# Kernel tuning notes

Measured on AMD Instinct MI355X. Metric: run time of the kernel, lower is better.

The kernel has to match this reference:

```python
import jax, jax.numpy as jnp
import numpy as np

EPS = 0.5          # residual scaling (module __init__ eps)
N = 100_000        # num nodes
E = 1_250_000      # num edges (avg degree ~12.5)
D = 64             # feature dim


def setup_inputs() -> dict:
    key = jax.random.key(0)
    k1, k2, k3 = jax.random.split(key, 3)
    x = jax.random.normal(k1, (N, D), dtype=jnp.float32)
    src = jax.random.randint(k2, (E,), 0, N, dtype=jnp.int32)
    dst = jax.random.randint(k3, (E,), 0, N, dtype=jnp.int32)
    return {"x": x, "src": src, "dst": dst}


def reference(x, src, dst):
    n = x.shape[0]
    # out-degree of each node = number of edges with that node as source
    deg = jax.ops.segment_sum(jnp.ones(src.shape, dtype=x.dtype), src, num_segments=n)
    norm = jnp.power(jnp.maximum(deg, 1.0), -0.5)          # [N]
    edge_norm = norm[src] * norm[dst]                      # [E] (u_mul_v)
    msg = x[src] * edge_norm[:, None]                      # [E, D] (u_mul_e)
    h = jax.ops.segment_sum(msg, dst, num_segments=n)      # sum per destination
    return h + x * EPS
```

## Files before the change

kernel.cpp:

```cpp
#include <hip/hip_runtime.h>

constexpr int D        = 64;
constexpr float EPS    = 0.5f;
constexpr int BKT      = 128;
constexpr int CAPB_MAX = 2048;
constexpr int EPB      = 4096;
constexpr int NBMAX    = 1024;
constexpr int MAXOVF   = 65536;

__device__ __forceinline__ unsigned int f2bf(float f) {
    unsigned int u = __float_as_uint(f);
    return (u + 0x7FFFu + ((u >> 16) & 1u)) >> 16;
}
__device__ __forceinline__ float bf2f_lo(unsigned int v) { return __uint_as_float(v << 16); }
__device__ __forceinline__ float bf2f_hi(unsigned int v) { return __uint_as_float(v & 0xFFFF0000u); }


__global__ void init_kernel(int* __restrict__ curD, int* __restrict__ curS,
                            int* __restrict__ ovf_cnt, int* __restrict__ sovf_cnt,
                            int NB, int capb) {
    int i = blockIdx.x * blockDim.x + threadIdx.x;
    if (i < NB) { curD[i] = i * capb; curS[i] = i * capb; }
    if (i == 0) { *ovf_cnt = 0; *sovf_cnt = 0; }
}

__global__ __launch_bounds__(256)
void partition_kernel(const int* __restrict__ src, const int* __restrict__ dst,
                      int* __restrict__ curD, int* __restrict__ curS,
                      unsigned int* __restrict__ rec, unsigned char* __restrict__ srec,
                      int* __restrict__ ovf_cnt, int* __restrict__ ovf,
                      int* __restrict__ sovf_cnt, int* __restrict__ sovf,
                      int E, int NB, int capb) {
    __shared__ int histD[NBMAX];
    __shared__ int histS[NBMAX];
    __shared__ int startD[NBMAX];
    __shared__ int startS[NBMAX];
    const int base = blockIdx.x * EPB;
    const int tid  = threadIdx.x;
    for (int b = tid; b < NB; b += 256) { histD[b] = 0; histS[b] = 0; }
    __syncthreads();

    #pragma unroll
    for (int k = 0; k < EPB / 256; ++k) {
        int e = base + tid + k * 256;
        if (e < E) {
            atomicAdd(&histD[dst[e] >> 7], 1);
            atomicAdd(&histS[src[e] >> 7], 1);
        }
    }
    __syncthreads();
    for (int b = tid; b < NB; b += 256) {
        int c = histD[b];
        startD[b] = (c > 0) ? atomicAdd(&curD[b], c) : 0;
        histD[b] = 0;
        int c2 = histS[b];
        startS[b] = (c2 > 0) ? atomicAdd(&curS[b], c2) : 0;
        histS[b] = 0;
    }
    __syncthreads();
    #pragma unroll
    for (int k = 0; k < EPB / 256; ++k) {
        int e = base + tid + k * 256;
        if (e < E) {
            int s = src[e], t = dst[e];
            int bD = t >> 7;
            int r  = atomicAdd(&histD[bD], 1);
            int pD = startD[bD] + r;
            if (pD < (bD + 1) * capb) {
                rec[pD] = ((unsigned int)s << 7) | (unsigned int)(t & (BKT - 1));
            } else {
                int i = atomicAdd(ovf_cnt, 1);
                if (i < MAXOVF) { ovf[2 * i] = s; ovf[2 * i + 1] = t; }
            }
            int bS = s >> 7;
            int r2 = atomicAdd(&histS[bS], 1);
            int pS = startS[bS] + r2;
            if (pS < (bS + 1) * capb) {
                srec[pS] = (unsigned char)(s & (BKT - 1));
            } else {
                int i = atomicAdd(sovf_cnt, 1);
                if (i < MAXOVF) sovf[i] = s;
            }
        }
    }
}

__global__ __launch_bounds__(256)
void combo_kernel(const unsigned int* __restrict__ rec, const unsigned char* __restrict__ srec,
                  const int* __restrict__ curD, const int* __restrict__ curS,
                  int* __restrict__ csr, int* __restrict__ row_start,
                  int* __restrict__ row_cnt, const float2* __restrict__ x2,
                  float* __restrict__ norm, unsigned int* __restrict__ yh,
                  const int* __restrict__ sovf_cnt, const int* __restrict__ sovf,
                  int n, int NB, int capb) {
    __shared__ unsigned int recs[CAPB_MAX];
    __shared__ int srcs[CAPB_MAX];
    __shared__ int hist[BKT];
    __shared__ int scanv[BKT];
    __shared__ int rankb[BKT];
    __shared__ float nrm[BKT];
    const int tid = threadIdx.x;

    if (blockIdx.x >= NB) {
        int b = blockIdx.x - NB;
        int cnt = curS[b] - b * capb;
        if (cnt > capb) cnt = capb;
        if (tid < BKT) hist[tid] = 0;
        __syncthreads();
        for (int i = tid; i < cnt; i += 256)
            atomicAdd(&hist[srec[(size_t)b * capb + i]], 1);
        __syncthreads();
        int oc = *sovf_cnt;
        if (oc > 0) {
            if (oc > MAXOVF) oc = MAXOVF;
            for (int i = tid; i < oc; i += 256) {
                int s = sovf[i];
                if ((s >> 7) == b) atomicAdd(&hist[s & (BKT - 1)], 1);
            }
            __syncthreads();
        }
        if (tid < BKT) {
            int node = b * BKT + tid;
            float nm = rsqrtf(fmaxf((float)hist[tid], 1.0f));
            nrm[tid] = nm;
            if (node < n) norm[node] = nm;
        }
        __syncthreads();
        int nodes = n - b * BKT;
        if (nodes > BKT) nodes = BKT;
        if (nodes < 0) nodes = 0;
        int total = nodes * (D / 2);
        size_t gbase = (size_t)b * BKT * (D / 2);
        for (int i = tid; i < total; i += 256) {
            float2 v = x2[gbase + i];
            float nm = nrm[i >> 5];
            yh[gbase + i] = f2bf(v.x * nm) | (f2bf(v.y * nm) << 16);
        }
        return;
    }

    const int b = blockIdx.x;
    int cnt = curD[b] - b * capb;
    if (cnt > capb) cnt = capb;
    for (int i = tid; i < cnt; i += 256) recs[i] = rec[(size_t)b * capb + i];
    if (tid < BKT) hist[tid] = 0;
    __syncthreads();
    for (int i = tid; i < cnt; i += 256) atomicAdd(&hist[recs[i] & (BKT - 1)], 1);
    __syncthreads();
    if (tid < BKT) scanv[tid] = hist[tid];
    __syncthreads();
    #pragma unroll
    for (int off = 1; off < BKT; off <<= 1) {
        int t = 0;
        if (tid < BKT && tid >= off) t = scanv[tid - off];
        __syncthreads();
        if (tid < BKT) scanv[tid] += t;
        __syncthreads();
    }
    if (tid < BKT) {
        int excl = scanv[tid] - hist[tid];
        rankb[tid] = excl;
        int node = b * BKT + tid;
        if (node < n) {
            row_start[node] = b * capb + excl;
            row_cnt[node]   = hist[tid];
        }
    }
    __syncthreads();
    for (int i = tid; i < cnt; i += 256) {
        unsigned int v = recs[i];
        int pos = atomicAdd(&rankb[v & (BKT - 1)], 1);
        srcs[pos] = (int)(v >> 7);
    }
    __syncthreads();
    for (int i = tid; i < cnt; i += 256) csr[(size_t)b * capb + i] = srcs[i];
}

__global__ __launch_bounds__(256)
void gather8_kernel(const uint4* __restrict__ yr4, const float4* __restrict__ x4,
                    const int* __restrict__ csr, const int* __restrict__ row_start,
                    const int* __restrict__ row_cnt, const float* __restrict__ norm,
                    float4* __restrict__ out4, int n) {
    int wid  = (blockIdx.x * blockDim.x + threadIdx.x) >> 6;
    int lane = threadIdx.x & 63;
    int fl   = lane & 7;
    int node = wid * 8 + (lane >> 3);
    bool valid = node < n;
    int rs  = valid ? row_start[node] : 0;
    int cnt = valid ? row_cnt[node] : 0;
    int m = cnt;
    m = max(m, __shfl_xor(m, 8));
    m = max(m, __shfl_xor(m, 16));
    m = max(m, __shfl_xor(m, 32));
    float a0 = 0.f, a1 = 0.f, a2 = 0.f, a3 = 0.f, a4 = 0.f, a5 = 0.f, a6 = 0.f, a7 = 0.f;
    for (int k = 0; k < m; k += 4) {
        #pragma unroll
        for (int j = 0; j < 4; ++j) {
            int kj = k + j;
            bool take = kj < cnt;
            int s = csr[rs + (take ? kj : 0)];
            s = take ? s : 0;
            uint4 v = yr4[(size_t)s * 8 + fl];
            if (!take) { v.x = 0u; v.y = 0u; v.z = 0u; v.w = 0u; }
            a0 += bf2f_lo(v.x); a1 += bf2f_hi(v.x);
            a2 += bf2f_lo(v.y); a3 += bf2f_hi(v.y);
            a4 += bf2f_lo(v.z); a5 += bf2f_hi(v.z);
            a6 += bf2f_lo(v.w); a7 += bf2f_hi(v.w);
        }
    }
    if (valid) {
        float nt = norm[node];
        size_t base = (size_t)node * 16 + fl * 2;
        float4 xv0 = x4[base], xv1 = x4[base + 1];
        float4 r0, r1;
        r0.x = a0 * nt + EPS * xv0.x;  r0.y = a1 * nt + EPS * xv0.y;
        r0.z = a2 * nt + EPS * xv0.z;  r0.w = a3 * nt + EPS * xv0.w;
        r1.x = a4 * nt + EPS * xv1.x;  r1.y = a5 * nt + EPS * xv1.y;
        r1.z = a6 * nt + EPS * xv1.z;  r1.w = a7 * nt + EPS * xv1.w;
        out4[base] = r0;
        out4[base + 1] = r1;
    }
}

__global__ void cleanup_kernel(const float* __restrict__ x, const float* __restrict__ norm,
                               const int* __restrict__ ovf_cnt, const int* __restrict__ ovf,
                               float* __restrict__ out) {
    int cnt = *ovf_cnt;
    if (cnt > MAXOVF) cnt = MAXOVF;
    long long total = (long long)cnt * D;
    long long stride = (long long)gridDim.x * blockDim.x;
    for (long long i = blockIdx.x * (long long)blockDim.x + threadIdx.x; i < total; i += stride) {
        int e = (int)(i >> 6), d = (int)(i & 63);
        int s = ovf[2 * e], t = ovf[2 * e + 1];
        atomicAdd(&out[(size_t)t * D + d], norm[s] * norm[t] * x[(size_t)s * D + d]);
    }
}


__global__ void fb_hist(const int* __restrict__ src, int* __restrict__ deg, int E) {
    int e = blockIdx.x * blockDim.x + threadIdx.x;
    if (e < E) atomicAdd(&deg[src[e]], 1);
}
__global__ void fb_norm(const int* __restrict__ deg, float* __restrict__ norm, int n) {
    int i = blockIdx.x * blockDim.x + threadIdx.x;
    if (i < n) norm[i] = rsqrtf(fmaxf((float)deg[i], 1.0f));
}
__global__ void fb_init_out(const float4* __restrict__ x, float4* __restrict__ out, int n4) {
    int i = blockIdx.x * blockDim.x + threadIdx.x;
    if (i < n4) {
        float4 v = x[i];
        out[i] = make_float4(v.x * EPS, v.y * EPS, v.z * EPS, v.w * EPS);
    }
}
__global__ void fb_scatter(const float* __restrict__ x, const int* __restrict__ src,
                           const int* __restrict__ dst, const float* __restrict__ norm,
                           float* __restrict__ out, int E) {
    long long tid = (long long)blockIdx.x * blockDim.x + threadIdx.x;
    int e = (int)(tid >> 6), d = (int)(tid & 63);
    if (e < E) {
        int s = src[e], t = dst[e];
        atomicAdd(&out[(size_t)t * D + d], norm[s] * norm[t] * x[(size_t)s * D + d]);
    }
}


extern "C" void kernel_launch(void* const* d_in, const int* in_sizes, int n_in,
                              void* d_out, int out_size, void* d_ws, size_t ws_size,
                              hipStream_t stream) {
    const float* x   = (const float*)d_in[0];
    const int*   src = (const int*)d_in[1];
    const int*   dst = (const int*)d_in[2];
    float* out = (float*)d_out;

    const int ND = in_sizes[0];
    const int E  = in_sizes[1];
    const int n  = ND / D;
    const int NB = (n + BKT - 1) / BKT;
    constexpr int B = 256;

    int capb = 0;
    for (int c : {2048, 1792}) {
        size_t need = (size_t)NB * c * 4
                    + (size_t)NB * c * 4
                    + (size_t)NB * c
                    + ((size_t)(2 * NB + 127) & ~63ull) * 4
                    + (size_t)n * 4 * 3
                    + (size_t)ND * 2
                    + (size_t)(128 + 3 * MAXOVF) * 4;
        if (need <= ws_size) { capb = c; break; }
    }

    if (NB <= NBMAX && capb > 0 && n < (1 << 24)) {
        unsigned int* rec   = (unsigned int*)d_ws;
        int*   csr          = (int*)(rec + (size_t)NB * capb);
        unsigned char* srec = (unsigned char*)(csr + (size_t)NB * capb);
        int*   curD         = (int*)(srec + (((size_t)NB * capb + 3) & ~3ull));
        int*   curS         = curD + NB;
        float* norm         = (float*)(curS + ((NB + 63) & ~63));
        int*   row_start    = (int*)(norm + n);
        int*   row_cnt      = row_start + n;
        unsigned int* yh    = (unsigned int*)(row_cnt + n);
        int*   ovf_cnt      = (int*)(yh + ND / 2);
        int*   sovf_cnt     = ovf_cnt + 64;
        int*   ovf          = sovf_cnt + 64;
        int*   sovf         = ovf + 2 * MAXOVF;

        init_kernel<<<(NB + B - 1) / B, B, 0, stream>>>(curD, curS, ovf_cnt, sovf_cnt, NB, capb);
        partition_kernel<<<(E + EPB - 1) / EPB, B, 0, stream>>>(src, dst, curD, curS, rec, srec,
                                                                ovf_cnt, ovf, sovf_cnt, sovf,
                                                                E, NB, capb);
        combo_kernel<<<2 * NB, B, 0, stream>>>(rec, srec, curD, curS, csr, row_start, row_cnt,
                                               (const float2*)x, norm, yh, sovf_cnt, sovf,
                                               n, NB, capb);
        gather8_kernel<<<(n + 31) / 32, B, 0, stream>>>((const uint4*)yh, (const float4*)x,
                                                        csr, row_start, row_cnt, norm,
                                                        (float4*)out, n);
        cleanup_kernel<<<64, B, 0, stream>>>(x, norm, ovf_cnt, ovf, out);
    } else {
        int*   deg  = (int*)d_ws;
        float* norm = (float*)d_ws + n;
        hipMemsetAsync(deg, 0, (size_t)n * sizeof(int), stream);
        fb_hist<<<(E + B - 1) / B, B, 0, stream>>>(src, deg, E);
        fb_norm<<<(n + B - 1) / B, B, 0, stream>>>(deg, norm, n);
        fb_init_out<<<(ND / 4 + B - 1) / B, B, 0, stream>>>((const float4*)x, (float4*)out, ND / 4);
        long long total = (long long)E * D;
        fb_scatter<<<(int)((total + B - 1) / B), B, 0, stream>>>(x, src, dst, norm, out, E);
    }
}
```

Before: 172.3 us.

## Fuse per-bucket sort with gather and compute degree via global atomics

Replaces the source-side byte-record partition and histogram with direct global atomicAdd into a per-node degree array. The per-bucket counting sort is fused with the aggregation into one 512-thread kernel that gathers from the sorted list held in shared memory, so the CSR, row_start and row_cnt arrays are never written to or read back from global memory. Edges per partition block are halved and the edge indices are kept in registers between passes, and norm is recomputed from deg where it is needed. The cost is up to 1.25M scattered global atomics for degree, and only NB (~782) blocks of 512 threads run the gather phase, which may limit memory-level parallelism.

```diff
diff --git a/kernel.cpp b/kernel.cpp
--- a/kernel.cpp
+++ b/kernel.cpp
@@ -4,7 +4,7 @@
 constexpr float EPS    = 0.5f;
 constexpr int BKT      = 128;
 constexpr int CAPB_MAX = 2048;
-constexpr int EPB      = 4096;
+constexpr int EPB      = 2048;
 constexpr int NBMAX    = 1024;
 constexpr int MAXOVF   = 65536;
 
@@ -16,36 +16,37 @@
 __device__ __forceinline__ float bf2f_hi(unsigned int v) { return __uint_as_float(v & 0xFFFF0000u); }
 
 
-__global__ void init_kernel(int* __restrict__ curD, int* __restrict__ curS,
-                            int* __restrict__ ovf_cnt, int* __restrict__ sovf_cnt,
-                            int NB, int capb) {
+__global__ void init_kernel(int* __restrict__ deg, int* __restrict__ curD,
+                            int* __restrict__ ovf_cnt, int n, int NB, int capb) {
     int i = blockIdx.x * blockDim.x + threadIdx.x;
-    if (i < NB) { curD[i] = i * capb; curS[i] = i * capb; }
-    if (i == 0) { *ovf_cnt = 0; *sovf_cnt = 0; }
+    if (i < n)  deg[i]  = 0;
+    if (i < NB) curD[i] = i * capb;
+    if (i == 0) *ovf_cnt = 0;
 }
 
 __global__ __launch_bounds__(256)
 void partition_kernel(const int* __restrict__ src, const int* __restrict__ dst,
-                      int* __restrict__ curD, int* __restrict__ curS,
-                      unsigned int* __restrict__ rec, unsigned char* __restrict__ srec,
+                      int* __restrict__ curD, unsigned int* __restrict__ rec,
+                      int* __restrict__ deg,
                       int* __restrict__ ovf_cnt, int* __restrict__ ovf,
-                      int* __restrict__ sovf_cnt, int* __restrict__ sovf,
                       int E, int NB, int capb) {
     __shared__ int histD[NBMAX];
-    __shared__ int histS[NBMAX];
     __shared__ int startD[NBMAX];
-    __shared__ int startS[NBMAX];
     const int base = blockIdx.x * EPB;
     const int tid  = threadIdx.x;
-    for (int b = tid; b < NB; b += 256) { histD[b] = 0; histS[b] = 0; }
-    __syncthreads();
-
+    for (int b = tid; b < NB; b += 256) histD[b] = 0;
+    __syncthreads();
+
+    int se[EPB / 256], te[EPB / 256];
     #pragma unroll
     for (int k = 0; k < EPB / 256; ++k) {
         int e = base + tid + k * 256;
+        se[k] = -1;
         if (e < E) {
-            atomicAdd(&histD[dst[e] >> 7], 1);
-            atomicAdd(&histS[src[e] >> 7], 1);
+            int s = src[e], t = dst[e];
+            se[k] = s; te[k] = t;
+            atomicAdd(&histD[t >> 7], 1);
+            atomicAdd(&deg[s], 1);
         }
     }
     __syncthreads();
@@ -53,16 +54,12 @@
         int c = histD[b];
         startD[b] = (c > 0) ? atomicAdd(&curD[b], c) : 0;
         histD[b] = 0;
-        int c2 = histS[b];
-        startS[b] = (c2 > 0) ? atomicAdd(&curS[b], c2) : 0;
-        histS[b] = 0;
     }
     __syncthreads();
     #pragma unroll
     for (int k = 0; k < EPB / 256; ++k) {
-        int e = base + tid + k * 256;
-        if (e < E) {
-            int s = src[e], t = dst[e];
+        if (se[k] >= 0) {
+            int s = se[k], t = te[k];
             int bD = t >> 7;
             int r  = atomicAdd(&histD[bD], 1);
             int pD = startD[bD] + r;
@@ -72,80 +69,54 @@
                 int i = atomicAdd(ovf_cnt, 1);
                 if (i < MAXOVF) { ovf[2 * i] = s; ovf[2 * i + 1] = t; }
             }
-            int bS = s >> 7;
-            int r2 = atomicAdd(&histS[bS], 1);
-            int pS = startS[bS] + r2;
-            if (pS < (bS + 1) * capb) {
-                srec[pS] = (unsigned char)(s & (BKT - 1));
-            } else {
-                int i = atomicAdd(sovf_cnt, 1);
-                if (i < MAXOVF) sovf[i] = s;
-            }
         }
     }
 }
 
 __global__ __launch_bounds__(256)
-void combo_kernel(const unsigned int* __restrict__ rec, const unsigned char* __restrict__ srec,
-                  const int* __restrict__ curD, const int* __restrict__ curS,
-                  int* __restrict__ csr, int* __restrict__ row_start,
-                  int* __restrict__ row_cnt, const float2* __restrict__ x2,
-                  float* __restrict__ norm, unsigned int* __restrict__ yh,
-                  const int* __restrict__ sovf_cnt, const int* __restrict__ sovf,
-                  int n, int NB, int capb) {
+void normyh_kernel(const int* __restrict__ deg, const float2* __restrict__ x2,
+                   unsigned int* __restrict__ yh, int n) {
+    const int b   = blockIdx.x;
+    const int tid = threadIdx.x;
+    __shared__ float nrm[BKT];
+    if (tid < BKT) {
+        int node = b * BKT + tid;
+        float dv = (node < n) ? (float)deg[node] : 1.0f;
+        nrm[tid] = rsqrtf(fmaxf(dv, 1.0f));
+    }
+    __syncthreads();
+    int nodes = n - b * BKT;
+    if (nodes > BKT) nodes = BKT;
+    if (nodes < 0) nodes = 0;
+    int total = nodes * (D / 2);
+    size_t gbase = (size_t)b * BKT * (D / 2);
+    for (int i = tid; i < total; i += 256) {
+        float2 v = x2[gbase + i];
+        float nm = nrm[i >> 5];
+        yh[gbase + i] = f2bf(v.x * nm) | (f2bf(v.y * nm) << 16);
+    }
+}
+
+__global__ __launch_bounds__(512)
+void sortgather_kernel(const unsigned int* __restrict__ rec, const int* __restrict__ curD,
+                       const int* __restrict__ deg, const uint4* __restrict__ yr4,
+                       const float4* __restrict__ x4, float4* __restrict__ out4,
+                       int n, int capb) {
     __shared__ unsigned int recs[CAPB_MAX];
     __shared__ int srcs[CAPB_MAX];
     __shared__ int hist[BKT];
     __shared__ int scanv[BKT];
     __shared__ int rankb[BKT];
-    __shared__ float nrm[BKT];
+    __shared__ int rsL[BKT];
+    const int b   = blockIdx.x;
     const int tid = threadIdx.x;
 
-    if (blockIdx.x >= NB) {
-        int b = blockIdx.x - NB;
-        int cnt = curS[b] - b * capb;
-        if (cnt > capb) cnt = capb;
-        if (tid < BKT) hist[tid] = 0;
-        __syncthreads();
-        for (int i = tid; i < cnt; i += 256)
-            atomicAdd(&hist[srec[(size_t)b * capb + i]], 1);
-        __syncthreads();
-        int oc = *sovf_cnt;
-        if (oc > 0) {
-            if (oc > MAXOVF) oc = MAXOVF;
-            for (int i = tid; i < oc; i += 256) {
-                int s = sovf[i];
-                if ((s >> 7) == b) atomicAdd(&hist[s & (BKT - 1)], 1);
-            }
-            __syncthreads();
-        }
-        if (tid < BKT) {
-            int node = b * BKT + tid;
-            float nm = rsqrtf(fmaxf((float)hist[tid], 1.0f));
-            nrm[tid] = nm;
-            if (node < n) norm[node] = nm;
-        }
-        __syncthreads();
-        int nodes = n - b * BKT;
-        if (nodes > BKT) nodes = BKT;
-        if (nodes < 0) nodes = 0;
-        int total = nodes * (D / 2);
-        size_t gbase = (size_t)b * BKT * (D / 2);
-        for (int i = tid; i < total; i += 256) {
-            float2 v = x2[gbase + i];
-            float nm = nrm[i >> 5];
-            yh[gbase + i] = f2bf(v.x * nm) | (f2bf(v.y * nm) << 16);
-        }
-        return;
-    }
-
-    const int b = blockIdx.x;
     int cnt = curD[b] - b * capb;
     if (cnt > capb) cnt = capb;
-    for (int i = tid; i < cnt; i += 256) recs[i] = rec[(size_t)b * capb + i];
+    for (int i = tid; i < cnt; i += 512) recs[i] = rec[(size_t)b * capb + i];
     if (tid < BKT) hist[tid] = 0;
     __syncthreads();
-    for (int i = tid; i < cnt; i += 256) atomicAdd(&hist[recs[i] & (BKT - 1)], 1);
+    for (int i = tid; i < cnt; i += 512) atomicAdd(&hist[recs[i] & (BKT - 1)], 1);
     __syncthreads();
     if (tid < BKT) scanv[tid] = hist[tid];
     __syncthreads();
@@ -160,69 +131,68 @@
     if (tid < BKT) {
         int excl = scanv[tid] - hist[tid];
         rankb[tid] = excl;
-        int node = b * BKT + tid;
-        if (node < n) {
-            row_start[node] = b * capb + excl;
-            row_cnt[node]   = hist[tid];
-        }
-    }
-    __syncthreads();
-    for (int i = tid; i < cnt; i += 256) {
+        rsL[tid]   = excl;
+    }
+    __syncthreads();
+    for (int i = tid; i < cnt; i += 512) {
         unsigned int v = recs[i];
         int pos = atomicAdd(&rankb[v & (BKT - 1)], 1);
         srcs[pos] = (int)(v >> 7);
     }
     __syncthreads();
-    for (int i = tid; i < cnt; i += 256) csr[(size_t)b * capb + i] = srcs[i];
-}
-
-__global__ __launch_bounds__(256)
-void gather8_kernel(const uint4* __restrict__ yr4, const float4* __restrict__ x4,
-                    const int* __restrict__ csr, const int* __restrict__ row_start,
-                    const int* __restrict__ row_cnt, const float* __restrict__ norm,
-                    float4* __restrict__ out4, int n) {
-    int wid  = (blockIdx.x * blockDim.x + threadIdx.x) >> 6;
-    int lane = threadIdx.x & 63;
-    int fl   = lane & 7;
-    int node = wid * 8 + (lane >> 3);
-    bool valid = node < n;
-    int rs  = valid ? row_start[node] : 0;
-    int cnt = valid ? row_cnt[node] : 0;
-    int m = cnt;
-    m = max(m, __shfl_xor(m, 8));
-    m = max(m, __shfl_xor(m, 16));
-    m = max(m, __shfl_xor(m, 32));
-    float a0 = 0.f, a1 = 0.f, a2 = 0.f, a3 = 0.f, a4 = 0.f, a5 = 0.f, a6 = 0.f, a7 = 0.f;
-    for (int k = 0; k < m; k += 4) {
-        #pragma unroll
-        for (int j = 0; j < 4; ++j) {
-            int kj = k + j;
-            bool take = kj < cnt;
-            int s = csr[rs + (take ? kj : 0)];
-            s = take ? s : 0;
-            uint4 v = yr4[(size_t)s * 8 + fl];
-            if (!take) { v.x = 0u; v.y = 0u; v.z = 0u; v.w = 0u; }
-            a0 += bf2f_lo(v.x); a1 += bf2f_hi(v.x);
-            a2 += bf2f_lo(v.y); a3 += bf2f_hi(v.y);
-            a4 += bf2f_lo(v.z); a5 += bf2f_hi(v.z);
-            a6 += bf2f_lo(v.w); a7 += bf2f_hi(v.w);
-        }
-    }
-    if (valid) {
-        float nt = norm[node];
-        size_t base = (size_t)node * 16 + fl * 2;
-        float4 xv0 = x4[base], xv1 = x4[base + 1];
-        float4 r0, r1;
-        r0.x = a0 * nt + EPS * xv0.x;  r0.y = a1 * nt + EPS * xv0.y;
-        r0.z = a2 * nt + EPS * xv0.z;  r0.w = a3 * nt + EPS * xv0.w;
-        r1.x = a4 * nt + EPS * xv1.x;  r1.y = a5 * nt + EPS * xv1.y;
-        r1.z = a6 * nt + EPS * xv1.z;  r1.w = a7 * nt + EPS * xv1.w;
-        out4[base] = r0;
-        out4[base + 1] = r1;
-    }
-}
-
-__global__ void cleanup_kernel(const float* __restrict__ x, const float* __restrict__ norm,
+
+    const int wave = tid >> 6;
+    const int lane = tid & 63;
+    const int fl   = lane & 7;
+    const int oct  = lane >> 3;
+    #pragma unroll
+    for (int r = 0; r < 2; ++r) {
+        int ln   = (r * 8 + wave) * 8 + oct;
+        int node = b * BKT + ln;
+        bool valid = node < n;
+        int rsl = valid ? rsL[ln]  : 0;
+        int cl  = valid ? hist[ln] : 0;
+        int m = cl;
+        m = max(m, __shfl_xor(m, 8));
+        m = max(m, __shfl_xor(m, 16));
+        m = max(m, __shfl_xor(m, 32));
+        float a0 = 0.f, a1 = 0.f, a2 = 0.f, a3 = 0.f;
+        float a4 = 0.f, a5 = 0.f, a6 = 0.f, a7 = 0.f;
+        for (int k = 0; k < m; k += 8) {
+            int sb[8];
+            #pragma unroll
+            for (int j = 0; j < 8; ++j) {
+                int kj = k + j;
+                sb[j] = (kj < cl) ? srcs[rsl + kj] : -1;
+            }
+            #pragma unroll
+            for (int j = 0; j < 8; ++j) {
+                bool take = sb[j] >= 0;
+                int s = take ? sb[j] : 0;
+                uint4 v = yr4[(size_t)s * 8 + fl];
+                if (!take) { v.x = 0u; v.y = 0u; v.z = 0u; v.w = 0u; }
+                a0 += bf2f_lo(v.x); a1 += bf2f_hi(v.x);
+                a2 += bf2f_lo(v.y); a3 += bf2f_hi(v.y);
+                a4 += bf2f_lo(v.z); a5 += bf2f_hi(v.z);
+                a6 += bf2f_lo(v.w); a7 += bf2f_hi(v.w);
+            }
+        }
+        if (valid) {
+            float nt = rsqrtf(fmaxf((float)deg[node], 1.0f));
+            size_t basei = (size_t)node * 16 + fl * 2;
+            float4 xv0 = x4[basei], xv1 = x4[basei + 1];
+            float4 r0, r1;
+            r0.x = a0 * nt + EPS * xv0.x;  r0.y = a1 * nt + EPS * xv0.y;
+            r0.z = a2 * nt + EPS * xv0.z;  r0.w = a3 * nt + EPS * xv0.w;
+            r1.x = a4 * nt + EPS * xv1.x;  r1.y = a5 * nt + EPS * xv1.y;
+            r1.z = a6 * nt + EPS * xv1.z;  r1.w = a7 * nt + EPS * xv1.w;
+            out4[basei] = r0;
+            out4[basei + 1] = r1;
+        }
+    }
+}
+
+__global__ void cleanup_kernel(const float* __restrict__ x, const int* __restrict__ deg,
                                const int* __restrict__ ovf_cnt, const int* __restrict__ ovf,
                                float* __restrict__ out) {
     int cnt = *ovf_cnt;
@@ -232,7 +202,9 @@
     for (long long i = blockIdx.x * (long long)blockDim.x + threadIdx.x; i < total; i += stride) {
         int e = (int)(i >> 6), d = (int)(i & 63);
         int s = ovf[2 * e], t = ovf[2 * e + 1];
-        atomicAdd(&out[(size_t)t * D + d], norm[s] * norm[t] * x[(size_t)s * D + d]);
+        float ns = rsqrtf(fmaxf((float)deg[s], 1.0f));
+        float nt = rsqrtf(fmaxf((float)deg[t], 1.0f));
+        atomicAdd(&out[(size_t)t * D + d], ns * nt * x[(size_t)s * D + d]);
     }
 }
 
@@ -281,41 +253,30 @@
     int capb = 0;
     for (int c : {2048, 1792}) {
         size_t need = (size_t)NB * c * 4
-                    + (size_t)NB * c * 4
-                    + (size_t)NB * c
-                    + ((size_t)(2 * NB + 127) & ~63ull) * 4
-                    + (size_t)n * 4 * 3
+                    + (size_t)((n + 3) & ~3) * 4
                     + (size_t)ND * 2
-                    + (size_t)(128 + 3 * MAXOVF) * 4;
+                    + (size_t)((NB + 63) & ~63) * 4
+                    + (size_t)(64 + 2 * MAXOVF) * 4;
         if (need <= ws_size) { capb = c; break; }
     }
 
     if (NB <= NBMAX && capb > 0 && n < (1 << 24)) {
-        unsigned int* rec   = (unsigned int*)d_ws;
-        int*   csr          = (int*)(rec + (size_t)NB * capb);
-        unsigned char* srec = (unsigned char*)(csr + (size_t)NB * capb);
-        int*   curD         = (int*)(srec + (((size_t)NB * capb + 3) & ~3ull));
-        int*   curS         = curD + NB;
-        float* norm         = (float*)(curS + ((NB + 63) & ~63));
-        int*   row_start    = (int*)(norm + n);
-        int*   row_cnt      = row_start + n;
-        unsigned int* yh    = (unsigned int*)(row_cnt + n);
-        int*   ovf_cnt      = (int*)(yh + ND / 2);
-        int*   sovf_cnt     = ovf_cnt + 64;
-        int*   ovf          = sovf_cnt + 64;
-        int*   sovf         = ovf + 2 * MAXOVF;
-
-        init_kernel<<<(NB + B - 1) / B, B, 0, stream>>>(curD, curS, ovf_cnt, sovf_cnt, NB, capb);
-        partition_kernel<<<(E + EPB - 1) / EPB, B, 0, stream>>>(src, dst, curD, curS, rec, srec,
-                                                                ovf_cnt, ovf, sovf_cnt, sovf,
-                                                                E, NB, capb);
-        combo_kernel<<<2 * NB, B, 0, stream>>>(rec, srec, curD, curS, csr, row_start, row_cnt,
-                                               (const float2*)x, norm, yh, sovf_cnt, sovf,
-                                               n, NB, capb);
-        gather8_kernel<<<(n + 31) / 32, B, 0, stream>>>((const uint4*)yh, (const float4*)x,
-                                                        csr, row_start, row_cnt, norm,
-                                                        (float4*)out, n);
-        cleanup_kernel<<<64, B, 0, stream>>>(x, norm, ovf_cnt, ovf, out);
+        unsigned int* rec = (unsigned int*)d_ws;
+        int* deg          = (int*)(rec + (size_t)NB * capb);
+        unsigned int* yh  = (unsigned int*)(deg + ((n + 3) & ~3));
+        int* curD         = (int*)(yh + ND / 2);
+        int* ovf_cnt      = curD + ((NB + 63) & ~63);
+        int* ovf          = ovf_cnt + 64;
+
+        int zmax  = (n > NB) ? n : NB;
+        int zgrid = (zmax + B - 1) / B;
+        init_kernel<<<zgrid, B, 0, stream>>>(deg, curD, ovf_cnt, n, NB, capb);
+        partition_kernel<<<(E + EPB - 1) / EPB, B, 0, stream>>>(src, dst, curD, rec, deg,
+                                                                ovf_cnt, ovf, E, NB, capb);
+        normyh_kernel<<<NB, B, 0, stream>>>(deg, (const float2*)x, yh, n);
+        sortgather_kernel<<<NB, 512, 0, stream>>>(rec, curD, deg, (const uint4*)yh,
+                                                  (const float4*)x, (float4*)out, n, capb);
+        cleanup_kernel<<<64, B, 0, stream>>>(x, deg, ovf_cnt, ovf, out);
     } else {
         int*   deg  = (int*)d_ws;
         float* norm = (float*)d_ws + n;
```

Measured after the change: 185.0 us. +7.3%, slower.
